# Kernel optimization log

Hardware: AMD Instinct MI355X
Metric: run time of the kernel (lower is better)

Reference implementation:

```python
import jax, jax.numpy as jnp
import numpy as np

B, M, H, D, K, V = 32, 4096, 32, 4096, 128, 128

def setup_inputs() -> dict:
    key = jax.random.key(0)
    ks = jax.random.split(key, 7)
    s = lambda fan: 1.0 / np.sqrt(fan)
    return {
        "x": jax.random.normal(ks[0], (B, D), jnp.float32),
        "K_prev": jax.random.normal(ks[1], (B, M, K), jnp.float32),
        "V_prev": jax.random.normal(ks[2], (B, M, V), jnp.float32),
        "P_q": jax.random.normal(ks[3], (H, D, K), jnp.float32) * s(D),
        "P_k": jax.random.normal(ks[4], (D, K), jnp.float32) * s(D),
        "P_v": jax.random.normal(ks[5], (D, V), jnp.float32) * s(D),
        "P_o": jax.random.normal(ks[6], (H, D, V), jnp.float32) * s(D),
    }

def reference(x, K_prev, V_prev, P_q, P_k, P_v, P_o):
    # per-head query projection: [b,d] x [h,d,k] -> [b,h,k]
    q = jnp.einsum('bd,hdk->bhk', x, P_q)
    # shared (multi-query) K/V projection of the new token, appended to cache
    k_new = jnp.einsum('bd,dk->bk', x, P_k)          # [b,k]
    v_new = jnp.einsum('bd,dv->bv', x, P_v)          # [b,v]
    K_new = jnp.concatenate([K_prev, k_new[:, None, :]], axis=1)  # [b,m+1,k]
    V_new = jnp.concatenate([V_prev, v_new[:, None, :]], axis=1)  # [b,m+1,v]
    # attention over shared cache
    logits = jnp.einsum('bhk,bmk->bhm', q, K_new)    # [b,h,m+1]
    w = jax.nn.softmax(logits, axis=-1)
    o = jnp.einsum('bhm,bmv->bhv', w, V_new)         # [b,h,v]
    y = jnp.einsum('bhv,hdv->bd', o, P_o)            # [b,d]
    return (y, K_new, V_new)
```

## Files before the change

### kernel.cpp

```cpp
#include <hip/hip_runtime.h>

#define B_ 32
#define M_ 4096
#define M1_ 4097
#define H_ 32
#define D_ 4096

typedef float float4_ __attribute__((ext_vector_type(4)));
typedef float f32x4 __attribute__((ext_vector_type(4)));
typedef short short8 __attribute__((ext_vector_type(8)));
typedef short short4_ __attribute__((ext_vector_type(4)));

#define KOFF 131072
#define VOFF 16912384

#define Q_OFF     0u
#define O_OFF     139264u
#define YPART_OFF 270336u
#define QPART_OFF 1318912u
#define APO_OFF   1318912u
#define MSUM_OFF  2367488u

#define WAITV(n) asm volatile("s_waitcnt vmcnt(" #n ")" ::: "memory")
#define SBAR() __builtin_amdgcn_sched_barrier(0)

__device__ __forceinline__ unsigned short f2bf(float f) {
  union { float f; unsigned u; } cv; cv.f = f;
  return (unsigned short)((cv.u + 0x7FFFu + ((cv.u >> 16) & 1u)) >> 16);
}
__device__ __forceinline__ float bf2f(unsigned short b) {
  union { unsigned u; float f; } cv; cv.u = ((unsigned)b) << 16;
  return cv.f;
}
__device__ __forceinline__ short8 pack8(const float* t) {
  short8 r;
#pragma unroll
  for (int j = 0; j < 8; ++j) r[j] = (short)f2bf(t[j]);
  return r;
}
__device__ __forceinline__ short8 load8cvt(const float* __restrict__ p) {
  float t[8];
  float4_ v0 = *(const float4_*)p;
  float4_ v1 = *(const float4_*)(p + 4);
#pragma unroll
  for (int j = 0; j < 4; ++j) { t[j] = v0[j]; t[4 + j] = v1[j]; }
  return pack8(t);
}
__device__ __forceinline__ void load_lds16(const float* g, float* l) {
  __builtin_amdgcn_global_load_lds(
      (const __attribute__((address_space(1))) unsigned int*)g,
      (__attribute__((address_space(3))) unsigned int*)l, 16, 0, 0);
}

__global__ __launch_bounds__(256) void k_proj(const float* __restrict__ x,
    const float* __restrict__ Pq, const float* __restrict__ Pk,
    const float* __restrict__ Pv, unsigned short* __restrict__ qpart)
{
  int bid = blockIdx.x;
  int hh = bid >> 5;
  int c  = bid & 31;
  const float* W = (hh < 32) ? (Pq + (size_t)hh * D_ * 128)
                             : ((hh == 32) ? Pk : Pv);
  int d0 = c * 128;
  int tid = threadIdx.x;
  int w = tid >> 6, l = tid & 63, l15 = l & 15, lg = l >> 4;
  f32x4 acc[2][2] = {};
  for (int ks = 0; ks < 4; ++ks) {
    int dk = d0 + ks * 32 + lg * 8;
    short8 af[2];
#pragma unroll
    for (int bt = 0; bt < 2; ++bt)
      af[bt] = load8cvt(x + (size_t)(bt * 16 + l15) * D_ + dk);
    short8 bf[2];
#pragma unroll
    for (int nti = 0; nti < 2; ++nti) {
      int col = (2 * w + nti) * 16 + l15;
      float t[8];
#pragma unroll
      for (int j = 0; j < 8; ++j) t[j] = W[(size_t)(dk + j) * 128 + col];
      bf[nti] = pack8(t);
    }
#pragma unroll
    for (int bt = 0; bt < 2; ++bt)
#pragma unroll
      for (int nti = 0; nti < 2; ++nti)
        acc[bt][nti] = __builtin_amdgcn_mfma_f32_16x16x32_bf16(af[bt], bf[nti], acc[bt][nti], 0, 0, 0);
  }
#pragma unroll
  for (int bt = 0; bt < 2; ++bt)
#pragma unroll
    for (int nti = 0; nti < 2; ++nti) {
      int k = (2 * w + nti) * 16 + l15;
#pragma unroll
      for (int i = 0; i < 4; ++i) {
        int b = bt * 16 + lg * 4 + i;
        qpart[(size_t)((c * 34 + hh) * 32 + b) * 128 + k] = f2bf(acc[bt][nti][i]);
      }
    }
}

__global__ __launch_bounds__(256) void k_reduce_q(const unsigned short* __restrict__ qpart,
    float* __restrict__ q, float* __restrict__ dout)
{
  int idx = blockIdx.x * 256 + threadIdx.x;
  if (idx >= 34 * 32 * 128) return;
  float s = 0.f;
#pragma unroll
  for (int cc = 0; cc < 32; ++cc) s += bf2f(qpart[(size_t)cc * 139264 + idx]);
  q[idx] = s;
  int hh = idx >> 12;
  if (hh >= 32) {
    int b = (idx >> 7) & 31, k = idx & 127;
    size_t off = (hh == 32) ? (size_t)KOFF : (size_t)VOFF;
    dout[off + ((size_t)b * M1_ + M_) * 128 + k] = s;
  }
}

#define ISSUE(T, KR, VB) do { \
  const float* Kc_ = Kb + (T) * 16 * 128; \
  const float* Vc_ = Vb + (T) * 16 * 128; \
  const float* Krow_ = Kc_ + (size_t)l15 * 128; \
  _Pragma("unroll") \
  for (int ks = 0; ks < 4; ++ks) { \
    KR[2 * ks]     = *(const float4_*)(Krow_ + ks * 32 + lg * 8); \
    KR[2 * ks + 1] = *(const float4_*)(Krow_ + ks * 32 + lg * 8 + 4); \
  } \
  _Pragma("unroll") \
  for (int i = 0; i < 8; ++i) load_lds16(Vc_ + i * 256 + l * 4, VB + i * 256); \
} while (0)

#define DO_CHUNK(T, KR, VB) do { \
   \
  float* Knrow_ = Knb + (T) * 16 * 128 + (size_t)l15 * 128; \
  _Pragma("unroll") \
  for (int ks = 0; ks < 4; ++ks) { \
    *(float4_*)(Knrow_ + ks * 32 + lg * 8)     = KR[2 * ks]; \
    *(float4_*)(Knrow_ + ks * 32 + lg * 8 + 4) = KR[2 * ks + 1]; \
  } \
   \
  float* Vnc_ = Vnb + (T) * 16 * 128; \
  _Pragma("unroll") \
  for (int i = 0; i < 8; ++i) { \
    float4_ t_ = *(const float4_*)(VB + (i * 64 + l) * 4); \
    *(float4_*)(Vnc_ + (size_t)(i * 64 + l) * 4) = t_; \
  } \
   \
  short8 kf_[4]; \
  _Pragma("unroll") \
  for (int ks = 0; ks < 4; ++ks) { \
    float tt_[8]; \
    _Pragma("unroll") \
    for (int j = 0; j < 4; ++j) { tt_[j] = KR[2 * ks][j]; tt_[4 + j] = KR[2 * ks + 1][j]; } \
    kf_[ks] = pack8(tt_); \
  } \
   \
  f32x4 sacc_[2] = {}; \
  _Pragma("unroll") \
  for (int ks = 0; ks < 4; ++ks) \
    _Pragma("unroll") \
    for (int ht = 0; ht < 2; ++ht) \
      sacc_[ht] = __builtin_amdgcn_mfma_f32_16x16x32_bf16(af[ht][ks], kf_[ks], sacc_[ht], 0, 0, 0); \
   \
  _Pragma("unroll") \
  for (int ht = 0; ht < 2; ++ht) { \
    f32x4 mx_; \
    _Pragma("unroll") \
    for (int i = 0; i < 4; ++i) { \
      float v_ = sacc_[ht][i]; \
      v_ = fmaxf(v_, __shfl_xor(v_, 1)); v_ = fmaxf(v_, __shfl_xor(v_, 2)); \
      v_ = fmaxf(v_, __shfl_xor(v_, 4)); v_ = fmaxf(v_, __shfl_xor(v_, 8)); \
      mx_[i] = v_; \
    } \
    f32x4 fsc_; \
    _Pragma("unroll") \
    for (int i = 0; i < 4; ++i) { \
      float mn_ = fmaxf(mrun[ht][i], mx_[i]); \
      fsc_[i] = __expf(mrun[ht][i] - mn_); \
      mrun[ht][i] = mn_; \
    } \
    _Pragma("unroll") \
    for (int vt = 0; vt < 8; ++vt) oacc[ht][vt] *= fsc_; \
    _Pragma("unroll") \
    for (int i = 0; i < 4; ++i) { \
      float p_ = __expf(sacc_[ht][i] - mrun[ht][i]); \
      lsum[ht][i] = lsum[ht][i] * fsc_[i] + p_; \
      Plds[w][ht * 16 + lg * 4 + i][l15] = f2bf(p_); \
    } \
  } \
  asm volatile("" ::: "memory"); \
   \
  short8 z_ = {}; \
  short8 pa_[2]; \
  _Pragma("unroll") \
  for (int ht = 0; ht < 2; ++ht) \
    pa_[ht] = (lg < 2) ? *(const short8*)&Plds[w][ht * 16 + l15][lg * 8] : z_; \
  _Pragma("unroll") \
  for (int vt = 0; vt < 8; ++vt) { \
    short8 bfv_ = z_; \
    if (lg < 2) { \
      float t_[8]; \
      _Pragma("unroll") \
      for (int j = 0; j < 8; ++j) t_[j] = VB[(lg * 8 + j) * 128 + vt * 16 + l15]; \
      bfv_ = pack8(t_); \
    } \
    _Pragma("unroll") \
    for (int ht = 0; ht < 2; ++ht) \
      oacc[ht][vt] = __builtin_amdgcn_mfma_f32_16x16x32_bf16(pa_[ht], bfv_, oacc[ht][vt], 0, 0, 0); \
  } \
} while (0)

__global__ __launch_bounds__(256, 2) void k_attn(const float* __restrict__ Kp,
    const float* __restrict__ Vp, const float* __restrict__ q,
    float* __restrict__ dout, unsigned short* __restrict__ apo,
    float* __restrict__ msum)
{
  __shared__ float Vbuf[4][2][2048];
  __shared__ unsigned short Plds[4][32][16];
  __shared__ float Mh[4][32], Sh[4][32];
  int bid = blockIdx.x;
  int b = bid >> 4;
  int tid = threadIdx.x, w = tid >> 6, l = tid & 63, l15 = l & 15, lg = l >> 4;
  int wid = (bid & 15) * 4 + w;
  const float* Kb = Kp + ((size_t)b * M_ + wid * 64) * 128;
  const float* Vb = Vp + ((size_t)b * M_ + wid * 64) * 128;
  float* Knb = dout + KOFF + ((size_t)b * M1_ + wid * 64) * 128;
  float* Vnb = dout + VOFF + ((size_t)b * M1_ + wid * 64) * 128;
  float* vb0 = &Vbuf[w][0][0];
  float* vb1 = &Vbuf[w][1][0];

  short8 af[2][4];
#pragma unroll
  for (int ks = 0; ks < 4; ++ks)
#pragma unroll
    for (int ht = 0; ht < 2; ++ht)
      af[ht][ks] = load8cvt(q + (size_t)((ht * 16 + l15) * 32 + b) * 128 + ks * 32 + lg * 8);

  float4_ krA[8], krB[8];
  f32x4 mrun[2], lsum[2], oacc[2][8];
#pragma unroll
  for (int ht = 0; ht < 2; ++ht) {
#pragma unroll
    for (int i = 0; i < 4; ++i) { mrun[ht][i] = -3e38f; lsum[ht][i] = 0.f; }
#pragma unroll
    for (int vt = 0; vt < 8; ++vt) oacc[ht][vt] = f32x4{0.f, 0.f, 0.f, 0.f};
  }

  ISSUE(0, krA, vb0); SBAR();
  ISSUE(1, krB, vb1); SBAR();
  WAITV(16); SBAR();
  DO_CHUNK(0, krA, vb0);
  ISSUE(2, krA, vb0); SBAR();
  WAITV(32); SBAR();
  DO_CHUNK(1, krB, vb1);
  ISSUE(3, krB, vb1); SBAR();
  WAITV(32); SBAR();
  DO_CHUNK(2, krA, vb0);
  WAITV(16); SBAR();
  DO_CHUNK(3, krB, vb1);

#pragma unroll
  for (int ht = 0; ht < 2; ++ht)
#pragma unroll
    for (int i = 0; i < 4; ++i) {
      float s = lsum[ht][i];
      s += __shfl_xor(s, 1); s += __shfl_xor(s, 2);
      s += __shfl_xor(s, 4); s += __shfl_xor(s, 8);
      lsum[ht][i] = s;
    }
  if (l15 == 0) {
#pragma unroll
    for (int ht = 0; ht < 2; ++ht)
#pragma unroll
      for (int i = 0; i < 4; ++i) {
        int h = ht * 16 + lg * 4 + i;
        Mh[w][h] = mrun[ht][i];
        Sh[w][h] = lsum[ht][i];
      }
  }
  __syncthreads();
  float* Ob = &Vbuf[w][0][0];
#pragma unroll
  for (int ht = 0; ht < 2; ++ht)
#pragma unroll
    for (int i = 0; i < 4; ++i) {
      int h = ht * 16 + lg * 4 + i;
      float ms = fmaxf(fmaxf(Mh[0][h], Mh[1][h]), fmaxf(Mh[2][h], Mh[3][h]));
      float f = __expf(mrun[ht][i] - ms);
#pragma unroll
      for (int vt = 0; vt < 8; ++vt)
        Ob[h * 128 + vt * 16 + l15] = oacc[ht][vt][i] * f;
    }
  __syncthreads();
  int blk = bid & 15;
  size_t sblk = ((size_t)b * 16 + blk) * 32;
  if (tid < 32) {
    int h = tid;
    float ms = fmaxf(fmaxf(Mh[0][h], Mh[1][h]), fmaxf(Mh[2][h], Mh[3][h]));
    float ss = Sh[0][h] * __expf(Mh[0][h] - ms) + Sh[1][h] * __expf(Mh[1][h] - ms)
             + Sh[2][h] * __expf(Mh[2][h] - ms) + Sh[3][h] * __expf(Mh[3][h] - ms);
    msum[(sblk + h) * 2]     = ms;
    msum[(sblk + h) * 2 + 1] = ss;
  }
  const float* Vall = &Vbuf[0][0][0];
  for (int idx = tid; idx < 4096; idx += 256) {
    float s = Vall[idx] + Vall[4096 + idx] + Vall[8192 + idx] + Vall[12288 + idx];
    apo[(sblk + (idx >> 7)) * 128 + (idx & 127)] = f2bf(s);
  }
}

__global__ __launch_bounds__(256) void k_combine(const unsigned short* __restrict__ apo,
    const float* __restrict__ msum, const float* __restrict__ q, float* __restrict__ o)
{
  __shared__ float redN[4][128];
  __shared__ float redD[4];
  int bid = blockIdx.x;
  int b = bid >> 5, h = bid & 31;
  int tid = threadIdx.x, w = tid >> 6, l = tid & 63;

  const float* qh = q + (size_t)(h * 32 + b) * 128;
  const float* kn = q + (size_t)(1024 + b) * 128;
  const float* vn = q + (size_t)(1056 + b) * 128;
  float e = qh[2 * l] * kn[2 * l] + qh[2 * l + 1] * kn[2 * l + 1];
#pragma unroll
  for (int d = 1; d < 64; d <<= 1) e += __shfl_xor(e, d);

  float gm = (l < 16) ? msum[((size_t)(b * 16 + l) * 32 + h) * 2] : -3e38f;
#pragma unroll
  for (int d = 1; d < 64; d <<= 1) gm = fmaxf(gm, __shfl_xor(gm, d));
  gm = fmaxf(gm, e);
  float pe = __expf(e - gm);

  float num0 = 0.f, num1 = 0.f, den = 0.f;
#pragma unroll
  for (int i = 0; i < 4; ++i) {
    int cc = w * 4 + i;
    size_t slot = (size_t)(b * 16 + cc) * 32 + h;
    float sc = __expf(msum[slot * 2] - gm);
    den += sc * msum[slot * 2 + 1];
    unsigned pp = *(const unsigned*)&apo[slot * 128 + l * 2];
    num0 += sc * bf2f((unsigned short)(pp & 0xFFFFu));
    num1 += sc * bf2f((unsigned short)(pp >> 16));
  }
  redN[w][l * 2] = num0;
  redN[w][l * 2 + 1] = num1;
  if (l == 0) redD[w] = den + (w == 0 ? pe : 0.f);
  __syncthreads();
  if (tid < 128) {
    float num = redN[0][tid] + redN[1][tid] + redN[2][tid] + redN[3][tid] + pe * vn[tid];
    float dd  = redD[0] + redD[1] + redD[2] + redD[3];
    o[((size_t)(b * 32 + h)) * 128 + tid] = num / dd;
  }
}

__global__ __launch_bounds__(256) void k_out(const float* __restrict__ o,
    const float* __restrict__ Po, float* __restrict__ ypart)
{
  int bid = blockIdx.x;
  int dt = bid >> 3, hg = bid & 7;
  int tid = threadIdx.x, w = tid >> 6, l = tid & 63, l15 = l & 15, lg = l >> 4;
  int d = dt * 64 + w * 16 + l15;
  f32x4 acc[2] = {};
  for (int hi = 0; hi < 4; ++hi) {
    int h = hg * 4 + hi;
#pragma unroll
    for (int ks = 0; ks < 4; ++ks) {
      short8 af[2];
#pragma unroll
      for (int bt = 0; bt < 2; ++bt)
        af[bt] = load8cvt(o + ((size_t)((bt * 16 + l15) * 32 + h)) * 128 + ks * 32 + lg * 8);
      short8 bf = load8cvt(Po + ((size_t)h * D_ + d) * 128 + ks * 32 + lg * 8);
#pragma unroll
      for (int bt = 0; bt < 2; ++bt)
        acc[bt] = __builtin_amdgcn_mfma_f32_16x16x32_bf16(af[bt], bf, acc[bt], 0, 0, 0);
    }
  }
#pragma unroll
  for (int bt = 0; bt < 2; ++bt)
#pragma unroll
    for (int i = 0; i < 4; ++i) {
      int b = bt * 16 + lg * 4 + i;
      ypart[((size_t)(hg * 32 + b)) * 4096 + d] = acc[bt][i];
    }
}

__global__ __launch_bounds__(256) void k_reduce_y(const float* __restrict__ ypart,
    float* __restrict__ dout)
{
  int idx = blockIdx.x * 256 + threadIdx.x;
  float s = 0.f;
#pragma unroll
  for (int g = 0; g < 8; ++g) s += ypart[(size_t)g * 131072 + idx];
  dout[idx] = s;
}

extern "C" void kernel_launch(void* const* d_in, const int* in_sizes, int n_in,
                              void* d_out, int out_size, void* d_ws, size_t ws_size,
                              hipStream_t stream) {
  (void)in_sizes; (void)n_in; (void)out_size; (void)ws_size;
  const float* x  = (const float*)d_in[0];
  const float* Kp = (const float*)d_in[1];
  const float* Vp = (const float*)d_in[2];
  const float* Pq = (const float*)d_in[3];
  const float* Pk = (const float*)d_in[4];
  const float* Pv = (const float*)d_in[5];
  const float* Po = (const float*)d_in[6];
  float* out = (float*)d_out;
  float* ws  = (float*)d_ws;
  float* q     = ws + Q_OFF;
  float* o     = ws + O_OFF;
  float* ypart = ws + YPART_OFF;
  unsigned short* qpart = (unsigned short*)(ws + QPART_OFF);
  unsigned short* apo   = (unsigned short*)(ws + APO_OFF);
  float* msum  = ws + MSUM_OFF;

  hipLaunchKernelGGL(k_proj,     dim3(1088), dim3(256), 0, stream, x, Pq, Pk, Pv, qpart);
  hipLaunchKernelGGL(k_reduce_q, dim3(544),  dim3(256), 0, stream, qpart, q, out);
  hipLaunchKernelGGL(k_attn,     dim3(512),  dim3(256), 0, stream, Kp, Vp, q, out, apo, msum);
  hipLaunchKernelGGL(k_combine,  dim3(1024), dim3(256), 0, stream, apo, msum, q, o);
  hipLaunchKernelGGL(k_out,      dim3(512),  dim3(256), 0, stream, o, Po, ypart);
  hipLaunchKernelGGL(k_reduce_y, dim3(512),  dim3(256), 0, stream, ypart, out);
}
```

Before: 127.4 us.

## Double attention grid with single-buffered LDS and halve projection split-K blocks

```diff
diff --git a/kernel.cpp b/kernel.cpp
--- a/kernel.cpp
+++ b/kernel.cpp
@@ -19,7 +19,7 @@
 #define YPART_OFF 270336u
 #define QPART_OFF 1318912u
 #define APO_OFF   1318912u
-#define MSUM_OFF  2367488u
+#define MSUM_OFF  3416064u
 
 #define WAITV(n) asm volatile("s_waitcnt vmcnt(" #n ")" ::: "memory")
 #define SBAR() __builtin_amdgcn_sched_barrier(0)
@@ -57,15 +57,15 @@
     const float* __restrict__ Pv, unsigned short* __restrict__ qpart)
 {
   int bid = blockIdx.x;
-  int hh = bid >> 5;
-  int c  = bid & 31;
+  int hh = bid >> 4;
+  int c  = bid & 15;
   const float* W = (hh < 32) ? (Pq + (size_t)hh * D_ * 128)
                              : ((hh == 32) ? Pk : Pv);
-  int d0 = c * 128;
+  int d0 = c * 256;
   int tid = threadIdx.x;
   int w = tid >> 6, l = tid & 63, l15 = l & 15, lg = l >> 4;
   f32x4 acc[2][2] = {};
-  for (int ks = 0; ks < 4; ++ks) {
+  for (int ks = 0; ks < 8; ++ks) {
     int dk = d0 + ks * 32 + lg * 8;
     short8 af[2];
 #pragma unroll
@@ -106,7 +106,7 @@
   if (idx >= 34 * 32 * 128) return;
   float s = 0.f;
 #pragma unroll
-  for (int cc = 0; cc < 32; ++cc) s += bf2f(qpart[(size_t)cc * 139264 + idx]);
+  for (int cc = 0; cc < 16; ++cc) s += bf2f(qpart[(size_t)cc * 139264 + idx]);
   q[idx] = s;
   int hh = idx >> 12;
   if (hh >= 32) {
@@ -116,35 +116,25 @@
   }
 }
 
-#define ISSUE(T, KR, VB) do { \
-  const float* Kc_ = Kb + (T) * 16 * 128; \
-  const float* Vc_ = Vb + (T) * 16 * 128; \
-  const float* Krow_ = Kc_ + (size_t)l15 * 128; \
+#define ISSUE_KV(T, KR) do { \
+  const float* Krow_ = Kb + (T) * 2048 + (size_t)l15 * 128; \
   _Pragma("unroll") \
   for (int ks = 0; ks < 4; ++ks) { \
     KR[2 * ks]     = *(const float4_*)(Krow_ + ks * 32 + lg * 8); \
     KR[2 * ks + 1] = *(const float4_*)(Krow_ + ks * 32 + lg * 8 + 4); \
   } \
+  const float* Vc_ = Vb + (T) * 2048; \
   _Pragma("unroll") \
   for (int i = 0; i < 8; ++i) load_lds16(Vc_ + i * 256 + l * 4, VB + i * 256); \
 } while (0)
 
-#define DO_CHUNK(T, KR, VB) do { \
-   \
-  float* Knrow_ = Knb + (T) * 16 * 128 + (size_t)l15 * 128; \
+#define CHUNK_QK(T, KR) do { \
+  float* Knrow_ = Knb + (T) * 2048 + (size_t)l15 * 128; \
   _Pragma("unroll") \
   for (int ks = 0; ks < 4; ++ks) { \
     *(float4_*)(Knrow_ + ks * 32 + lg * 8)     = KR[2 * ks]; \
     *(float4_*)(Knrow_ + ks * 32 + lg * 8 + 4) = KR[2 * ks + 1]; \
   } \
-   \
-  float* Vnc_ = Vnb + (T) * 16 * 128; \
-  _Pragma("unroll") \
-  for (int i = 0; i < 8; ++i) { \
-    float4_ t_ = *(const float4_*)(VB + (i * 64 + l) * 4); \
-    *(float4_*)(Vnc_ + (size_t)(i * 64 + l) * 4) = t_; \
-  } \
-   \
   short8 kf_[4]; \
   _Pragma("unroll") \
   for (int ks = 0; ks < 4; ++ks) { \
@@ -153,14 +143,12 @@
     for (int j = 0; j < 4; ++j) { tt_[j] = KR[2 * ks][j]; tt_[4 + j] = KR[2 * ks + 1][j]; } \
     kf_[ks] = pack8(tt_); \
   } \
-   \
   f32x4 sacc_[2] = {}; \
   _Pragma("unroll") \
   for (int ks = 0; ks < 4; ++ks) \
     _Pragma("unroll") \
     for (int ht = 0; ht < 2; ++ht) \
       sacc_[ht] = __builtin_amdgcn_mfma_f32_16x16x32_bf16(af[ht][ks], kf_[ks], sacc_[ht], 0, 0, 0); \
-   \
   _Pragma("unroll") \
   for (int ht = 0; ht < 2; ++ht) { \
     f32x4 mx_; \
@@ -188,7 +176,9 @@
     } \
   } \
   asm volatile("" ::: "memory"); \
-   \
+} while (0)
+
+#define CHUNK_PV(T) do { \
   short8 z_ = {}; \
   short8 pa_[2]; \
   _Pragma("unroll") \
@@ -207,26 +197,30 @@
     for (int ht = 0; ht < 2; ++ht) \
       oacc[ht][vt] = __builtin_amdgcn_mfma_f32_16x16x32_bf16(pa_[ht], bfv_, oacc[ht][vt], 0, 0, 0); \
   } \
+  float* Vnc_ = Vnb + (T) * 2048; \
+  _Pragma("unroll") \
+  for (int i = 0; i < 8; ++i) { \
+    float4_ t_ = *(const float4_*)(VB + (i * 64 + l) * 4); \
+    *(float4_*)(Vnc_ + (size_t)(i * 64 + l) * 4) = t_; \
+  } \
 } while (0)
 
-__global__ __launch_bounds__(256, 2) void k_attn(const float* __restrict__ Kp,
+__global__ __launch_bounds__(256, 3) void k_attn(const float* __restrict__ Kp,
     const float* __restrict__ Vp, const float* __restrict__ q,
     float* __restrict__ dout, unsigned short* __restrict__ apo,
     float* __restrict__ msum)
 {
-  __shared__ float Vbuf[4][2][2048];
+  __shared__ float Vbuf[4][2048];
   __shared__ unsigned short Plds[4][32][16];
   __shared__ float Mh[4][32], Sh[4][32];
   int bid = blockIdx.x;
-  int b = bid >> 4;
+  int b = bid >> 5, g = bid & 31;
   int tid = threadIdx.x, w = tid >> 6, l = tid & 63, l15 = l & 15, lg = l >> 4;
-  int wid = (bid & 15) * 4 + w;
-  const float* Kb = Kp + ((size_t)b * M_ + wid * 64) * 128;
-  const float* Vb = Vp + ((size_t)b * M_ + wid * 64) * 128;
-  float* Knb = dout + KOFF + ((size_t)b * M1_ + wid * 64) * 128;
-  float* Vnb = dout + VOFF + ((size_t)b * M1_ + wid * 64) * 128;
-  float* vb0 = &Vbuf[w][0][0];
-  float* vb1 = &Vbuf[w][1][0];
+  const float* Kb = Kp + ((size_t)b * M_ + g * 128 + w * 32) * 128;
+  const float* Vb = Vp + ((size_t)b * M_ + g * 128 + w * 32) * 128;
+  float* Knb = dout + KOFF + ((size_t)b * M1_ + g * 128 + w * 32) * 128;
+  float* Vnb = dout + VOFF + ((size_t)b * M1_ + g * 128 + w * 32) * 128;
+  float* VB = &Vbuf[w][0];
 
   short8 af[2][4];
 #pragma unroll
@@ -235,7 +229,7 @@
     for (int ht = 0; ht < 2; ++ht)
       af[ht][ks] = load8cvt(q + (size_t)((ht * 16 + l15) * 32 + b) * 128 + ks * 32 + lg * 8);
 
-  float4_ krA[8], krB[8];
+  float4_ kr[8];
   f32x4 mrun[2], lsum[2], oacc[2][8];
 #pragma unroll
   for (int ht = 0; ht < 2; ++ht) {
@@ -245,18 +239,17 @@
     for (int vt = 0; vt < 8; ++vt) oacc[ht][vt] = f32x4{0.f, 0.f, 0.f, 0.f};
   }
 
-  ISSUE(0, krA, vb0); SBAR();
-  ISSUE(1, krB, vb1); SBAR();
-  WAITV(16); SBAR();
-  DO_CHUNK(0, krA, vb0);
-  ISSUE(2, krA, vb0); SBAR();
-  WAITV(32); SBAR();
-  DO_CHUNK(1, krB, vb1);
-  ISSUE(3, krB, vb1); SBAR();
-  WAITV(32); SBAR();
-  DO_CHUNK(2, krA, vb0);
-  WAITV(16); SBAR();
-  DO_CHUNK(3, krB, vb1);
+  ISSUE_KV(0, kr); SBAR();
+  WAITV(8); SBAR();
+  CHUNK_QK(0, kr);
+  WAITV(8); SBAR();
+  CHUNK_PV(0);
+  SBAR();
+  ISSUE_KV(1, kr); SBAR();
+  WAITV(8); SBAR();
+  CHUNK_QK(1, kr);
+  WAITV(8); SBAR();
+  CHUNK_PV(1);
 
 #pragma unroll
   for (int ht = 0; ht < 2; ++ht)
@@ -278,7 +271,7 @@
       }
   }
   __syncthreads();
-  float* Ob = &Vbuf[w][0][0];
+  unsigned short* ObU = (unsigned short*)&Vbuf[w][0];
 #pragma unroll
   for (int ht = 0; ht < 2; ++ht)
 #pragma unroll
@@ -288,23 +281,22 @@
       float f = __expf(mrun[ht][i] - ms);
 #pragma unroll
       for (int vt = 0; vt < 8; ++vt)
-        Ob[h * 128 + vt * 16 + l15] = oacc[ht][vt][i] * f;
+        ObU[h * 128 + vt * 16 + l15] = f2bf(oacc[ht][vt][i] * f);
     }
   __syncthreads();
-  int blk = bid & 15;
-  size_t sblk = ((size_t)b * 16 + blk) * 32;
+  int slotbase = (b * 32 + g) * 32;
   if (tid < 32) {
     int h = tid;
     float ms = fmaxf(fmaxf(Mh[0][h], Mh[1][h]), fmaxf(Mh[2][h], Mh[3][h]));
     float ss = Sh[0][h] * __expf(Mh[0][h] - ms) + Sh[1][h] * __expf(Mh[1][h] - ms)
              + Sh[2][h] * __expf(Mh[2][h] - ms) + Sh[3][h] * __expf(Mh[3][h] - ms);
-    msum[(sblk + h) * 2]     = ms;
-    msum[(sblk + h) * 2 + 1] = ss;
-  }
-  const float* Vall = &Vbuf[0][0][0];
+    msum[(size_t)(slotbase + h) * 2]     = ms;
+    msum[(size_t)(slotbase + h) * 2 + 1] = ss;
+  }
+  const unsigned short* VU = (const unsigned short*)&Vbuf[0][0];
   for (int idx = tid; idx < 4096; idx += 256) {
-    float s = Vall[idx] + Vall[4096 + idx] + Vall[8192 + idx] + Vall[12288 + idx];
-    apo[(sblk + (idx >> 7)) * 128 + (idx & 127)] = f2bf(s);
+    float s = bf2f(VU[idx]) + bf2f(VU[4096 + idx]) + bf2f(VU[8192 + idx]) + bf2f(VU[12288 + idx]);
+    apo[(size_t)(slotbase + (idx >> 7)) * 128 + (idx & 127)] = f2bf(s);
   }
 }
 
@@ -324,7 +316,7 @@
 #pragma unroll
   for (int d = 1; d < 64; d <<= 1) e += __shfl_xor(e, d);
 
-  float gm = (l < 16) ? msum[((size_t)(b * 16 + l) * 32 + h) * 2] : -3e38f;
+  float gm = (l < 32) ? msum[((size_t)(b * 32 + l) * 32 + h) * 2] : -3e38f;
 #pragma unroll
   for (int d = 1; d < 64; d <<= 1) gm = fmaxf(gm, __shfl_xor(gm, d));
   gm = fmaxf(gm, e);
@@ -332,9 +324,9 @@
 
   float num0 = 0.f, num1 = 0.f, den = 0.f;
 #pragma unroll
-  for (int i = 0; i < 4; ++i) {
-    int cc = w * 4 + i;
-    size_t slot = (size_t)(b * 16 + cc) * 32 + h;
+  for (int i = 0; i < 8; ++i) {
+    int cc = w * 8 + i;
+    size_t slot = (size_t)(b * 32 + cc) * 32 + h;
     float sc = __expf(msum[slot * 2] - gm);
     den += sc * msum[slot * 2 + 1];
     unsigned pp = *(const unsigned*)&apo[slot * 128 + l * 2];
@@ -413,9 +405,9 @@
   unsigned short* apo   = (unsigned short*)(ws + APO_OFF);
   float* msum  = ws + MSUM_OFF;
 
-  hipLaunchKernelGGL(k_proj,     dim3(1088), dim3(256), 0, stream, x, Pq, Pk, Pv, qpart);
+  hipLaunchKernelGGL(k_proj,     dim3(544),  dim3(256), 0, stream, x, Pq, Pk, Pv, qpart);
   hipLaunchKernelGGL(k_reduce_q, dim3(544),  dim3(256), 0, stream, qpart, q, out);
-  hipLaunchKernelGGL(k_attn,     dim3(512),  dim3(256), 0, stream, Kp, Vp, q, out, apo, msum);
+  hipLaunchKernelGGL(k_attn,     dim3(1024), dim3(256), 0, stream, Kp, Vp, q, out, apo, msum);
   hipLaunchKernelGGL(k_combine,  dim3(1024), dim3(256), 0, stream, apo, msum, q, o);
   hipLaunchKernelGGL(k_out,      dim3(512),  dim3(256), 0, stream, o, Po, ypart);
   hipLaunchKernelGGL(k_reduce_y, dim3(512),  dim3(256), 0, stream, ypart, out);
```

Measured after the change: 135.2 us. 6.1% more time.

## Use nontemporal loads/stores for streamed data and halve projection split-K

Applied to the files above, without the earlier changes.

```diff
diff --git a/kernel.cpp b/kernel.cpp
--- a/kernel.cpp
+++ b/kernel.cpp
@@ -19,7 +19,7 @@
 #define YPART_OFF 270336u
 #define QPART_OFF 1318912u
 #define APO_OFF   1318912u
-#define MSUM_OFF  2367488u
+#define MSUM_OFF  2433024u
 
 #define WAITV(n) asm volatile("s_waitcnt vmcnt(" #n ")" ::: "memory")
 #define SBAR() __builtin_amdgcn_sched_barrier(0)
@@ -46,6 +46,23 @@
   for (int j = 0; j < 4; ++j) { t[j] = v0[j]; t[4 + j] = v1[j]; }
   return pack8(t);
 }
+__device__ __forceinline__ float4_ ntld4(const float* p) {
+  return __builtin_nontemporal_load((const float4_*)p);
+}
+__device__ __forceinline__ float ntldf(const float* p) {
+  return __builtin_nontemporal_load(p);
+}
+__device__ __forceinline__ void ntst4(float* p, float4_ v) {
+  __builtin_nontemporal_store(v, (float4_*)p);
+}
+__device__ __forceinline__ short8 load8cvt_nt(const float* __restrict__ p) {
+  float t[8];
+  float4_ v0 = ntld4(p);
+  float4_ v1 = ntld4(p + 4);
+#pragma unroll
+  for (int j = 0; j < 4; ++j) { t[j] = v0[j]; t[4 + j] = v1[j]; }
+  return pack8(t);
+}
 __device__ __forceinline__ void load_lds16(const float* g, float* l) {
   __builtin_amdgcn_global_load_lds(
       (const __attribute__((address_space(1))) unsigned int*)g,
@@ -57,15 +74,15 @@
     const float* __restrict__ Pv, unsigned short* __restrict__ qpart)
 {
   int bid = blockIdx.x;
-  int hh = bid >> 5;
-  int c  = bid & 31;
+  int hh = bid >> 4;
+  int c  = bid & 15;
   const float* W = (hh < 32) ? (Pq + (size_t)hh * D_ * 128)
                              : ((hh == 32) ? Pk : Pv);
-  int d0 = c * 128;
+  int d0 = c * 256;
   int tid = threadIdx.x;
   int w = tid >> 6, l = tid & 63, l15 = l & 15, lg = l >> 4;
   f32x4 acc[2][2] = {};
-  for (int ks = 0; ks < 4; ++ks) {
+  for (int ks = 0; ks < 8; ++ks) {
     int dk = d0 + ks * 32 + lg * 8;
     short8 af[2];
 #pragma unroll
@@ -77,7 +94,7 @@
       int col = (2 * w + nti) * 16 + l15;
       float t[8];
 #pragma unroll
-      for (int j = 0; j < 8; ++j) t[j] = W[(size_t)(dk + j) * 128 + col];
+      for (int j = 0; j < 8; ++j) t[j] = ntldf(&W[(size_t)(dk + j) * 128 + col]);
       bf[nti] = pack8(t);
     }
 #pragma unroll
@@ -94,7 +111,8 @@
 #pragma unroll
       for (int i = 0; i < 4; ++i) {
         int b = bt * 16 + lg * 4 + i;
-        qpart[(size_t)((c * 34 + hh) * 32 + b) * 128 + k] = f2bf(acc[bt][nti][i]);
+        __builtin_nontemporal_store(f2bf(acc[bt][nti][i]),
+            &qpart[(size_t)((c * 34 + hh) * 32 + b) * 128 + k]);
       }
     }
 }
@@ -106,13 +124,14 @@
   if (idx >= 34 * 32 * 128) return;
   float s = 0.f;
 #pragma unroll
-  for (int cc = 0; cc < 32; ++cc) s += bf2f(qpart[(size_t)cc * 139264 + idx]);
+  for (int cc = 0; cc < 16; ++cc)
+    s += bf2f(__builtin_nontemporal_load(&qpart[(size_t)cc * 139264 + idx]));
   q[idx] = s;
   int hh = idx >> 12;
   if (hh >= 32) {
     int b = (idx >> 7) & 31, k = idx & 127;
     size_t off = (hh == 32) ? (size_t)KOFF : (size_t)VOFF;
-    dout[off + ((size_t)b * M1_ + M_) * 128 + k] = s;
+    __builtin_nontemporal_store(s, &dout[off + ((size_t)b * M1_ + M_) * 128 + k]);
   }
 }
 
@@ -122,8 +141,8 @@
   const float* Krow_ = Kc_ + (size_t)l15 * 128; \
   _Pragma("unroll") \
   for (int ks = 0; ks < 4; ++ks) { \
-    KR[2 * ks]     = *(const float4_*)(Krow_ + ks * 32 + lg * 8); \
-    KR[2 * ks + 1] = *(const float4_*)(Krow_ + ks * 32 + lg * 8 + 4); \
+    KR[2 * ks]     = ntld4(Krow_ + ks * 32 + lg * 8); \
+    KR[2 * ks + 1] = ntld4(Krow_ + ks * 32 + lg * 8 + 4); \
   } \
   _Pragma("unroll") \
   for (int i = 0; i < 8; ++i) load_lds16(Vc_ + i * 256 + l * 4, VB + i * 256); \
@@ -134,15 +153,15 @@
   float* Knrow_ = Knb + (T) * 16 * 128 + (size_t)l15 * 128; \
   _Pragma("unroll") \
   for (int ks = 0; ks < 4; ++ks) { \
-    *(float4_*)(Knrow_ + ks * 32 + lg * 8)     = KR[2 * ks]; \
-    *(float4_*)(Knrow_ + ks * 32 + lg * 8 + 4) = KR[2 * ks + 1]; \
+    ntst4(Knrow_ + ks * 32 + lg * 8,     KR[2 * ks]); \
+    ntst4(Knrow_ + ks * 32 + lg * 8 + 4, KR[2 * ks + 1]); \
   } \
    \
   float* Vnc_ = Vnb + (T) * 16 * 128; \
   _Pragma("unroll") \
   for (int i = 0; i < 8; ++i) { \
     float4_ t_ = *(const float4_*)(VB + (i * 64 + l) * 4); \
-    *(float4_*)(Vnc_ + (size_t)(i * 64 + l) * 4) = t_; \
+    ntst4(Vnc_ + (size_t)(i * 64 + l) * 4, t_); \
   } \
    \
   short8 kf_[4]; \
@@ -304,7 +323,7 @@
   const float* Vall = &Vbuf[0][0][0];
   for (int idx = tid; idx < 4096; idx += 256) {
     float s = Vall[idx] + Vall[4096 + idx] + Vall[8192 + idx] + Vall[12288 + idx];
-    apo[(sblk + (idx >> 7)) * 128 + (idx & 127)] = f2bf(s);
+    __builtin_nontemporal_store(f2bf(s), &apo[(sblk + (idx >> 7)) * 128 + (idx & 127)]);
   }
 }
 
@@ -337,7 +356,7 @@
     size_t slot = (size_t)(b * 16 + cc) * 32 + h;
     float sc = __expf(msum[slot * 2] - gm);
     den += sc * msum[slot * 2 + 1];
-    unsigned pp = *(const unsigned*)&apo[slot * 128 + l * 2];
+    unsigned pp = __builtin_nontemporal_load((const unsigned*)&apo[slot * 128 + l * 2]);
     num0 += sc * bf2f((unsigned short)(pp & 0xFFFFu));
     num1 += sc * bf2f((unsigned short)(pp >> 16));
   }
@@ -368,7 +387,7 @@
 #pragma unroll
       for (int bt = 0; bt < 2; ++bt)
         af[bt] = load8cvt(o + ((size_t)((bt * 16 + l15) * 32 + h)) * 128 + ks * 32 + lg * 8);
-      short8 bf = load8cvt(Po + ((size_t)h * D_ + d) * 128 + ks * 32 + lg * 8);
+      short8 bf = load8cvt_nt(Po + ((size_t)h * D_ + d) * 128 + ks * 32 + lg * 8);
 #pragma unroll
       for (int bt = 0; bt < 2; ++bt)
         acc[bt] = __builtin_amdgcn_mfma_f32_16x16x32_bf16(af[bt], bf, acc[bt], 0, 0, 0);
@@ -379,7 +398,8 @@
 #pragma unroll
     for (int i = 0; i < 4; ++i) {
       int b = bt * 16 + lg * 4 + i;
-      ypart[((size_t)(hg * 32 + b)) * 4096 + d] = acc[bt][i];
+      __builtin_nontemporal_store(acc[bt][i],
+          &ypart[((size_t)(hg * 32 + b)) * 4096 + d]);
     }
 }
 
@@ -389,7 +409,8 @@
   int idx = blockIdx.x * 256 + threadIdx.x;
   float s = 0.f;
 #pragma unroll
-  for (int g = 0; g < 8; ++g) s += ypart[(size_t)g * 131072 + idx];
+  for (int g = 0; g < 8; ++g)
+    s += __builtin_nontemporal_load(&ypart[(size_t)g * 131072 + idx]);
   dout[idx] = s;
 }
 
@@ -413,7 +434,7 @@
   unsigned short* apo   = (unsigned short*)(ws + APO_OFF);
   float* msum  = ws + MSUM_OFF;
 
-  hipLaunchKernelGGL(k_proj,     dim3(1088), dim3(256), 0, stream, x, Pq, Pk, Pv, qpart);
+  hipLaunchKernelGGL(k_proj,     dim3(544),  dim3(256), 0, stream, x, Pq, Pk, Pv, qpart);
   hipLaunchKernelGGL(k_reduce_q, dim3(544),  dim3(256), 0, stream, qpart, q, out);
   hipLaunchKernelGGL(k_attn,     dim3(512),  dim3(256), 0, stream, Kp, Vp, q, out, apo, msum);
   hipLaunchKernelGGL(k_combine,  dim3(1024), dim3(256), 0, stream, apo, msum, q, o);
```

Measured after the change: 126.3 us. About the same (-0.9%).
